# Kernel optimization log

Hardware: AMD Instinct MI355X
Metric: run time of the kernel (lower is better)

The kernel has to match this reference:

```python
import jax, jax.numpy as jnp
import numpy as np

B, D, L = 2048, 4096, 3
# Fixed 5-node star graph hardcoded in the source module
SRC = jnp.array([1, 2, 3, 4])
DST = jnp.array([0, 0, 0, 0])


def setup_inputs() -> dict:
    key = jax.random.key(0)
    ks = jax.random.split(key, 13)
    inp = {}
    names = ["pair_now", "person_1_now", "person_2_now", "scene_now",
             "pair_pre", "person_1_pre", "person_2_pre", "scene_pre"]
    for i, n in enumerate(names):
        inp[n] = jax.random.normal(ks[i], (B, D), dtype=jnp.float32)
    # GatedGraphConv per-layer message weight [L, D, D]
    inp["W"] = jax.random.normal(ks[8], (L, D, D), dtype=jnp.float32) * 0.02
    # GRUCell parameters (torch layout: [3D, D] for ih and hh, biases [3D])
    inp["w_ih"] = jax.random.normal(ks[9], (3 * D, D), dtype=jnp.float32) * 0.02
    inp["w_hh"] = jax.random.normal(ks[10], (3 * D, D), dtype=jnp.float32) * 0.02
    inp["b_ih"] = jax.random.normal(ks[11], (3 * D,), dtype=jnp.float32) * 0.02
    inp["b_hh"] = jax.random.normal(ks[12], (3 * D,), dtype=jnp.float32) * 0.02
    return inp


def _forward(pair_now, person_1_now, person_2_now, scene_now,
             pair_pre, person_1_pre, person_2_pre, scene_pre,
             W, w_ih, w_hh, b_ih, b_hh):
    # mean over batch dim -> one D-vector per stream
    pre_means = jnp.stack([pair_pre.mean(0), person_1_pre.mean(0),
                           person_2_pre.mean(0), scene_pre.mean(0)])  # [4, D]
    now_means = jnp.stack([pair_now.mean(0), person_1_now.mean(0),
                           person_2_now.mean(0), scene_now.mean(0)])  # [4, D]

    def ggc(node0):
        # node features: [node0, pair_pre, p1_pre, p2_pre, scene_pre] -> [5, D]
        h = jnp.concatenate([node0[None], pre_means], axis=0)

        def step(h, Wl):
            msg = h @ Wl                                   # [5, D]
            agg = jnp.zeros_like(h).at[DST].add(msg[SRC])  # star: sum into node 0
            # torch GRUCell
            gi = agg @ w_ih.T + b_ih                       # [5, 3D]
            gh = h @ w_hh.T + b_hh
            i_r, i_z, i_n = jnp.split(gi, 3, axis=-1)
            h_r, h_z, h_n = jnp.split(gh, 3, axis=-1)
            r = jax.nn.sigmoid(i_r + h_r)
            z = jax.nn.sigmoid(i_z + h_z)
            n = jnp.tanh(i_n + r * h_n)
            return (1.0 - z) * n + z * h, None

        h, _ = jax.lax.scan(step, h, W)
        return h[0]  # node-0 output [D]

    outs = jax.vmap(ggc)(now_means)                 # [4, D]
    losses = jnp.mean((outs - pre_means) ** 2, -1)  # MSE per stream
    return jnp.sum(losses) * 10.0


def reference(pair_now, person_1_now, person_2_now, scene_now,
              pair_pre, person_1_pre, person_2_pre, scene_pre,
              W, w_ih, w_hh, b_ih, b_hh):
    return _forward(pair_now, person_1_now, person_2_now, scene_now,
                    pair_pre, person_1_pre, person_2_pre, scene_pre,
                    W, w_ih, w_hh, b_ih, b_hh)
```

## Files before the change

kernel.cpp:

```cpp
#include <hip/hip_runtime.h>
#include <hip/hip_bf16.h>

#define B  2048
#define D  4096
#define D3 12288
#define L  3
#define BK 256

struct Ptrs8 { const float* p[8]; };

typedef float          f32x4 __attribute__((ext_vector_type(4)));
typedef unsigned int   u32x2 __attribute__((ext_vector_type(2)));
typedef unsigned short u16x4 __attribute__((ext_vector_type(4)));

__device__ __forceinline__ f32x4 ldnt4(const float* p) {
    return __builtin_nontemporal_load(reinterpret_cast<const f32x4*>(p));
}
__device__ __forceinline__ f32x4 ld4(const float* p) {
    return *reinterpret_cast<const f32x4*>(p);
}
__device__ __forceinline__ void gload16(const void* g, void* l) {
    __builtin_amdgcn_global_load_lds(
        (const __attribute__((address_space(1))) unsigned int*)g,
        (__attribute__((address_space(3))) unsigned int*)l, 16, 0, 0);
}

__device__ __forceinline__ unsigned short f2bf(float f) {
    union { float f; unsigned int u; } v; v.f = f;
    unsigned int r = v.u + 0x7FFFu + ((v.u >> 16) & 1u);
    return (unsigned short)(r >> 16);
}
__device__ __forceinline__ float bf_lo(unsigned int u) {
    union { unsigned int u; float f; } v; v.u = u << 16; return v.f;
}
__device__ __forceinline__ float bf_hi(unsigned int u) {
    union { unsigned int u; float f; } v; v.u = u & 0xFFFF0000u; return v.f;
}

__global__ void k_mean_partial(Ptrs8 in, float* __restrict__ partials) {
    const int cc = blockIdx.x, rc = blockIdx.y, m = blockIdx.z;
    const float* __restrict__ src = in.p[m];
    const int col0 = cc * 1024 + threadIdx.x * 4;
    const size_t base = (size_t)(rc * 32) * D + col0;
    f32x4 a0 = {0,0,0,0}, a1 = {0,0,0,0}, a2 = {0,0,0,0}, a3 = {0,0,0,0};
    #pragma unroll
    for (int r = 0; r < 32; r += 4) {
        a0 += ldnt4(src + base + (size_t)(r + 0) * D);
        a1 += ldnt4(src + base + (size_t)(r + 1) * D);
        a2 += ldnt4(src + base + (size_t)(r + 2) * D);
        a3 += ldnt4(src + base + (size_t)(r + 3) * D);
    }
    const f32x4 acc = (a0 + a1) + (a2 + a3);
    *reinterpret_cast<f32x4*>(partials + ((size_t)(m * 64 + rc)) * D + col0) = acc;
}

__global__ void k_mean_finalize(const float* __restrict__ partials,
                                float* __restrict__ means,
                                float* __restrict__ h,
                                float* __restrict__ svec) {
    const int d = blockIdx.x * 256 + threadIdx.x;
    float mv[8];
    #pragma unroll
    for (int m = 0; m < 8; ++m) {
        float s = 0.f;
        for (int rc = 0; rc < 64; ++rc) s += partials[(size_t)(m * 64 + rc) * D + d];
        mv[m] = s * (1.0f / (float)B);
        means[m * D + d] = mv[m];
    }
    float ssum = 0.f;
    #pragma unroll
    for (int j = 0; j < 4; ++j) {
        h[j * D + d] = mv[4 + j];
        ssum += mv[4 + j];
    }
    #pragma unroll
    for (int s = 0; s < 4; ++s)
        h[(4 + s) * D + d] = mv[s];
    svec[d] = ssum;
}

__global__ void k_aggmsg_partial(const float* __restrict__ Wl,
                                 const float* __restrict__ svec,
                                 float* __restrict__ partials) {
    const int col0 = blockIdx.x * 1024 + threadIdx.x * 4;
    const int row0 = blockIdx.y * 16;
    f32x4 a0 = {0,0,0,0}, a1 = {0,0,0,0}, a2 = {0,0,0,0}, a3 = {0,0,0,0};
    #pragma unroll
    for (int r = 0; r < 16; r += 4) {
        a0 += svec[row0 + r + 0] * ldnt4(Wl + (size_t)(row0 + r + 0) * D + col0);
        a1 += svec[row0 + r + 1] * ldnt4(Wl + (size_t)(row0 + r + 1) * D + col0);
        a2 += svec[row0 + r + 2] * ldnt4(Wl + (size_t)(row0 + r + 2) * D + col0);
        a3 += svec[row0 + r + 3] * ldnt4(Wl + (size_t)(row0 + r + 3) * D + col0);
    }
    const f32x4 acc = (a0 + a1) + (a2 + a3);
    *reinterpret_cast<f32x4*>(partials + (size_t)blockIdx.y * D + col0) = acc;
}

__global__ void k_aggmsg_reduce(const float* __restrict__ partials,
                                float* __restrict__ aggmsg) {
    const int d = blockIdx.x * 256 + threadIdx.x;
    float s = 0.f;
    for (int r = 0; r < 256; ++r) s += partials[(size_t)r * D + d];
    aggmsg[d] = s;
}

__global__ __launch_bounds__(256)
void k_gates_f32(const float* __restrict__ w_ih,
                 const float* __restrict__ w_hh,
                 const float* __restrict__ h,
                 const float* __restrict__ aggmsg,
                 const float* __restrict__ b_ih,
                 const float* __restrict__ b_hh,
                 float* __restrict__ gi0,
                 float* __restrict__ gh,
                 unsigned short* __restrict__ wih_bf,
                 unsigned short* __restrict__ whh_bf) {
    __shared__ float sw[2][16][BK];
    const bool is_ih = (blockIdx.x >= 768);
    const int  kbase = (is_ih ? blockIdx.x - 768 : blockIdx.x) * 16;
    const float* __restrict__ wsrc = is_ih ? w_ih : w_hh;
    unsigned short* __restrict__ wdst = is_ih ? wih_bf : whh_bf;
    const int wid = threadIdx.x >> 6, lane = threadIdx.x & 63;

    auto stage = [&](int t, int b) {
        #pragma unroll
        for (int rr = 0; rr < 4; ++rr) {
            const int row = wid * 4 + rr;
            gload16(wsrc + (size_t)(kbase + row) * D + t * BK + lane * 4,
                    &sw[b][row][0]);
        }
    };

    float acc[4][8] = {};
    stage(0, 0);
    __syncthreads();
    for (int t = 0; t < 16; ++t) {
        if (t + 1 < 16) stage(t + 1, (t + 1) & 1);
        const int cb = t & 1;
        f32x4 wreg[4];
        #pragma unroll
        for (int rr = 0; rr < 4; ++rr) {
            const int row = wid * 4 + rr;
            wreg[rr] = *reinterpret_cast<const f32x4*>(&sw[cb][row][lane * 4]);
            u16x4 wb;
            wb.x = f2bf(wreg[rr].x); wb.y = f2bf(wreg[rr].y);
            wb.z = f2bf(wreg[rr].z); wb.w = f2bf(wreg[rr].w);
            *reinterpret_cast<u16x4*>(
                wdst + (size_t)(kbase + row) * D + t * BK + lane * 4) = wb;
        }
        if (!is_ih) {
            #pragma unroll
            for (int j = 0; j < 8; ++j) {
                const f32x4 hv = ld4(h + j * D + t * BK + lane * 4);
                #pragma unroll
                for (int rr = 0; rr < 4; ++rr)
                    acc[rr][j] += wreg[rr].x * hv.x + wreg[rr].y * hv.y
                                + wreg[rr].z * hv.z + wreg[rr].w * hv.w;
            }
        } else {
            const f32x4 av = ld4(aggmsg + t * BK + lane * 4);
            #pragma unroll
            for (int rr = 0; rr < 4; ++rr)
                acc[rr][0] += wreg[rr].x * av.x + wreg[rr].y * av.y
                            + wreg[rr].z * av.z + wreg[rr].w * av.w;
        }
        __syncthreads();
    }

    if (!is_ih) {
        #pragma unroll
        for (int rr = 0; rr < 4; ++rr)
            #pragma unroll
            for (int j = 0; j < 8; ++j) {
                float v = acc[rr][j];
                #pragma unroll
                for (int off = 32; off; off >>= 1) v += __shfl_xor(v, off);
                if (lane == 0)
                    gh[(size_t)j * D3 + kbase + wid * 4 + rr] = v + b_hh[kbase + wid * 4 + rr];
            }
    } else {
        #pragma unroll
        for (int rr = 0; rr < 4; ++rr) {
            float v = acc[rr][0];
            #pragma unroll
            for (int off = 32; off; off >>= 1) v += __shfl_xor(v, off);
            if (lane == 0)
                gi0[kbase + wid * 4 + rr] = v + b_ih[kbase + wid * 4 + rr];
        }
    }
}

__global__ __launch_bounds__(256)
void k_gates_bf(const unsigned short* __restrict__ wih_bf,
                const unsigned short* __restrict__ whh_bf,
                const float* __restrict__ h,
                const float* __restrict__ aggmsg,
                const float* __restrict__ b_ih,
                const float* __restrict__ b_hh,
                float* __restrict__ gi0,
                float* __restrict__ gh) {
    __shared__ unsigned short sw[2][16][BK];
    const bool is_ih = (blockIdx.x >= 768);
    const int  kbase = (is_ih ? blockIdx.x - 768 : blockIdx.x) * 16;
    const unsigned short* __restrict__ wsrc = is_ih ? wih_bf : whh_bf;
    const int wid = threadIdx.x >> 6, lane = threadIdx.x & 63;

    auto stage = [&](int t, int b) {
        #pragma unroll
        for (int c = 0; c < 2; ++c) {
            const int row = wid * 4 + c * 2;
            gload16(wsrc + (size_t)(kbase + row + (lane >> 5)) * D
                         + t * BK + (lane & 31) * 8,
                    &sw[b][row][0]);
        }
    };

    float acc[4][8] = {};
    stage(0, 0);
    __syncthreads();
    for (int t = 0; t < 16; ++t) {
        if (t + 1 < 16) stage(t + 1, (t + 1) & 1);
        const int cb = t & 1;
        float wf[4][4];
        #pragma unroll
        for (int rr = 0; rr < 4; ++rr) {
            const u32x2 wu = *reinterpret_cast<const u32x2*>(
                &sw[cb][wid * 4 + rr][lane * 4]);
            wf[rr][0] = bf_lo(wu.x); wf[rr][1] = bf_hi(wu.x);
            wf[rr][2] = bf_lo(wu.y); wf[rr][3] = bf_hi(wu.y);
        }
        if (!is_ih) {
            #pragma unroll
            for (int j = 0; j < 8; ++j) {
                const f32x4 hv = ld4(h + j * D + t * BK + lane * 4);
                #pragma unroll
                for (int rr = 0; rr < 4; ++rr)
                    acc[rr][j] += wf[rr][0] * hv.x + wf[rr][1] * hv.y
                                + wf[rr][2] * hv.z + wf[rr][3] * hv.w;
            }
        } else {
            const f32x4 av = ld4(aggmsg + t * BK + lane * 4);
            #pragma unroll
            for (int rr = 0; rr < 4; ++rr)
                acc[rr][0] += wf[rr][0] * av.x + wf[rr][1] * av.y
                            + wf[rr][2] * av.z + wf[rr][3] * av.w;
        }
        __syncthreads();
    }

    if (!is_ih) {
        #pragma unroll
        for (int rr = 0; rr < 4; ++rr)
            #pragma unroll
            for (int j = 0; j < 8; ++j) {
                float v = acc[rr][j];
                #pragma unroll
                for (int off = 32; off; off >>= 1) v += __shfl_xor(v, off);
                if (lane == 0)
                    gh[(size_t)j * D3 + kbase + wid * 4 + rr] = v + b_hh[kbase + wid * 4 + rr];
            }
    } else {
        #pragma unroll
        for (int rr = 0; rr < 4; ++rr) {
            float v = acc[rr][0];
            #pragma unroll
            for (int off = 32; off; off >>= 1) v += __shfl_xor(v, off);
            if (lane == 0)
                gi0[kbase + wid * 4 + rr] = v + b_ih[kbase + wid * 4 + rr];
        }
    }
}

__device__ __forceinline__ float sigmoidf_(float x) {
    return 1.0f / (1.0f + __expf(-x));
}

__global__ void k_gru(const float* __restrict__ gi0,
                      const float* __restrict__ gh,
                      const float* __restrict__ b_ih,
                      float* __restrict__ h,
                      float* __restrict__ svec) {
    const int d = blockIdx.x * 256 + threadIdx.x;
    const float bir = b_ih[d], biz = b_ih[D + d], bin = b_ih[2 * D + d];
    const float gir = gi0[d],  giz = gi0[D + d],  gin = gi0[2 * D + d];
    float ssum = 0.f;
    #pragma unroll
    for (int j = 0; j < 8; ++j) {
        const float ir = (j < 4) ? bir : gir;
        const float iz = (j < 4) ? biz : giz;
        const float in = (j < 4) ? bin : gin;
        const float hr = gh[(size_t)j * D3 + d];
        const float hz = gh[(size_t)j * D3 + D + d];
        const float hn = gh[(size_t)j * D3 + 2 * D + d];
        const float hv = h[j * D + d];
        const float r = sigmoidf_(ir + hr);
        const float z = sigmoidf_(iz + hz);
        const float n = tanhf(in + r * hn);
        const float hnew = (1.f - z) * n + z * hv;
        h[j * D + d] = hnew;
        if (j < 4) ssum += hnew;
    }
    svec[d] = ssum;
}

__global__ void k_loss(const float* __restrict__ h,
                       const float* __restrict__ means,
                       float* __restrict__ out) {
    __shared__ float red[4];
    float acc = 0.f;
    for (int idx = threadIdx.x; idx < 4 * D; idx += 256) {
        const int s = idx >> 12;
        const int d = idx & (D - 1);
        const float diff = h[(4 + s) * D + d] - means[(4 + s) * D + d];
        acc += diff * diff;
    }
    #pragma unroll
    for (int off = 32; off; off >>= 1) acc += __shfl_xor(acc, off);
    const int wave = threadIdx.x >> 6, lane = threadIdx.x & 63;
    if (lane == 0) red[wave] = acc;
    __syncthreads();
    if (threadIdx.x == 0)
        out[0] = (red[0] + red[1] + red[2] + red[3]) * (10.0f / (float)D);
}

extern "C" void kernel_launch(void* const* d_in, const int* in_sizes, int n_in,
                              void* d_out, int out_size, void* d_ws, size_t ws_size,
                              hipStream_t stream) {
    const float* W    = (const float*)d_in[8];
    const float* w_ih = (const float*)d_in[9];
    const float* w_hh = (const float*)d_in[10];
    const float* b_ih = (const float*)d_in[11];
    const float* b_hh = (const float*)d_in[12];

    float* ws     = (float*)d_ws;
    float* mpart  = ws;
    float* means  = mpart  + 8 * 64 * D;
    float* h      = means  + 8 * D;
    float* svec   = h      + 8 * D;
    float* apart  = svec   + D;
    float* aggmsg = apart  + 256 * D;
    float* gi0    = aggmsg + D;
    float* gh     = gi0    + D3;
    float* wbase  = gh     + 8 * D3;
    unsigned short* wih_bf = (unsigned short*)wbase;
    unsigned short* whh_bf = wih_bf + (size_t)D3 * D;

    Ptrs8 in8;
    for (int i = 0; i < 8; ++i) in8.p[i] = (const float*)d_in[i];

    k_mean_partial<<<dim3(4, 64, 8), 256, 0, stream>>>(in8, mpart);
    k_mean_finalize<<<16, 256, 0, stream>>>(mpart, means, h, svec);

    for (int l = 0; l < L; ++l) {
        const float* Wl = W + (size_t)l * D * D;
        k_aggmsg_partial<<<dim3(4, 256), 256, 0, stream>>>(Wl, svec, apart);
        k_aggmsg_reduce<<<16, 256, 0, stream>>>(apart, aggmsg);
        if (l == 0)
            k_gates_f32<<<1536, 256, 0, stream>>>(w_ih, w_hh, h, aggmsg,
                                                  b_ih, b_hh, gi0, gh,
                                                  wih_bf, whh_bf);
        else
            k_gates_bf<<<1536, 256, 0, stream>>>(wih_bf, whh_bf, h, aggmsg,
                                                 b_ih, b_hh, gi0, gh);
        k_gru<<<16, 256, 0, stream>>>(gi0, gh, b_ih, h, svec);
    }

    k_loss<<<1, 256, 0, stream>>>(h, means, (float*)d_out);
}
```

Before: 397.5 us.

## Restructure GRU gate GEMV kernels to direct register loads with rebalanced work split

Replaces the LDS double-buffered staging (global_load_lds plus __syncthreads) in both gate kernels with direct vector loads of weights into registers. w_hh blocks now cover 8 rows with each wave handling 2 of the 8 batch vectors, and w_ih rows get their own 384 blocks of 32 rows, for a grid of 1920. The bf16 kernel reads 8 bf16 values per lane per load, and conversion uses the HIP __float22bfloat162_rn intrinsic. The goal is to remove barrier and LDS overhead and rebalance the ih and hh halves. In exchange, the h vectors and w_hh rows are re-read by every wave, which adds cache traffic.

```diff
diff --git a/kernel.cpp b/kernel.cpp
--- a/kernel.cpp
+++ b/kernel.cpp
@@ -5,13 +5,12 @@
 #define D  4096
 #define D3 12288
 #define L  3
-#define BK 256
 
 struct Ptrs8 { const float* p[8]; };
 
 typedef float          f32x4 __attribute__((ext_vector_type(4)));
 typedef unsigned int   u32x2 __attribute__((ext_vector_type(2)));
-typedef unsigned short u16x4 __attribute__((ext_vector_type(4)));
+typedef unsigned int   u32x4 __attribute__((ext_vector_type(4)));
 
 __device__ __forceinline__ f32x4 ldnt4(const float* p) {
     return __builtin_nontemporal_load(reinterpret_cast<const f32x4*>(p));
@@ -19,22 +18,20 @@
 __device__ __forceinline__ f32x4 ld4(const float* p) {
     return *reinterpret_cast<const f32x4*>(p);
 }
-__device__ __forceinline__ void gload16(const void* g, void* l) {
-    __builtin_amdgcn_global_load_lds(
-        (const __attribute__((address_space(1))) unsigned int*)g,
-        (__attribute__((address_space(3))) unsigned int*)l, 16, 0, 0);
-}
-
-__device__ __forceinline__ unsigned short f2bf(float f) {
-    union { float f; unsigned int u; } v; v.f = f;
-    unsigned int r = v.u + 0x7FFFu + ((v.u >> 16) & 1u);
-    return (unsigned short)(r >> 16);
-}
 __device__ __forceinline__ float bf_lo(unsigned int u) {
     union { unsigned int u; float f; } v; v.u = u << 16; return v.f;
 }
 __device__ __forceinline__ float bf_hi(unsigned int u) {
     union { unsigned int u; float f; } v; v.u = u & 0xFFFF0000u; return v.f;
+}
+__device__ __forceinline__ void st_bf16x4(unsigned short* dst, f32x4 w) {
+    __hip_bfloat162 p0 = __float22bfloat162_rn(make_float2(w.x, w.y));
+    __hip_bfloat162 p1 = __float22bfloat162_rn(make_float2(w.z, w.w));
+    unsigned int u0, u1;
+    __builtin_memcpy(&u0, &p0, 4);
+    __builtin_memcpy(&u1, &p1, 4);
+    u32x2 v; v.x = u0; v.y = u1;
+    *reinterpret_cast<u32x2*>(dst) = v;
 }
 
 __global__ void k_mean_partial(Ptrs8 in, float* __restrict__ partials) {
@@ -115,77 +112,63 @@
                  float* __restrict__ gh,
                  unsigned short* __restrict__ wih_bf,
                  unsigned short* __restrict__ whh_bf) {
-    __shared__ float sw[2][16][BK];
-    const bool is_ih = (blockIdx.x >= 768);
-    const int  kbase = (is_ih ? blockIdx.x - 768 : blockIdx.x) * 16;
-    const float* __restrict__ wsrc = is_ih ? w_ih : w_hh;
-    unsigned short* __restrict__ wdst = is_ih ? wih_bf : whh_bf;
     const int wid = threadIdx.x >> 6, lane = threadIdx.x & 63;
-
-    auto stage = [&](int t, int b) {
+    if (blockIdx.x < 1536) {
+        const int kbase = blockIdx.x * 8;
+        const int j0 = wid * 2;
+        float acc[8][2] = {};
+        for (int i = 0; i < 16; ++i) {
+            const int idx = i * 256 + lane * 4;
+            const f32x4 hv0 = ld4(h + j0 * D + idx);
+            const f32x4 hv1 = ld4(h + (j0 + 1) * D + idx);
+            f32x4 w[8];
+            #pragma unroll
+            for (int r = 0; r < 8; ++r)
+                w[r] = ld4(w_hh + (size_t)(kbase + r) * D + idx);
+            st_bf16x4(whh_bf + (size_t)(kbase + j0) * D + idx, w[j0]);
+            st_bf16x4(whh_bf + (size_t)(kbase + j0 + 1) * D + idx, w[j0 + 1]);
+            #pragma unroll
+            for (int r = 0; r < 8; ++r) {
+                acc[r][0] += w[r].x * hv0.x + w[r].y * hv0.y
+                           + w[r].z * hv0.z + w[r].w * hv0.w;
+                acc[r][1] += w[r].x * hv1.x + w[r].y * hv1.y
+                           + w[r].z * hv1.z + w[r].w * hv1.w;
+            }
+        }
         #pragma unroll
-        for (int rr = 0; rr < 4; ++rr) {
-            const int row = wid * 4 + rr;
-            gload16(wsrc + (size_t)(kbase + row) * D + t * BK + lane * 4,
-                    &sw[b][row][0]);
-        }
-    };
-
-    float acc[4][8] = {};
-    stage(0, 0);
-    __syncthreads();
-    for (int t = 0; t < 16; ++t) {
-        if (t + 1 < 16) stage(t + 1, (t + 1) & 1);
-        const int cb = t & 1;
-        f32x4 wreg[4];
-        #pragma unroll
-        for (int rr = 0; rr < 4; ++rr) {
-            const int row = wid * 4 + rr;
-            wreg[rr] = *reinterpret_cast<const f32x4*>(&sw[cb][row][lane * 4]);
-            u16x4 wb;
-            wb.x = f2bf(wreg[rr].x); wb.y = f2bf(wreg[rr].y);
-            wb.z = f2bf(wreg[rr].z); wb.w = f2bf(wreg[rr].w);
-            *reinterpret_cast<u16x4*>(
-                wdst + (size_t)(kbase + row) * D + t * BK + lane * 4) = wb;
-        }
-        if (!is_ih) {
-            #pragma unroll
-            for (int j = 0; j < 8; ++j) {
-                const f32x4 hv = ld4(h + j * D + t * BK + lane * 4);
-                #pragma unroll
-                for (int rr = 0; rr < 4; ++rr)
-                    acc[rr][j] += wreg[rr].x * hv.x + wreg[rr].y * hv.y
-                                + wreg[rr].z * hv.z + wreg[rr].w * hv.w;
-            }
-        } else {
-            const f32x4 av = ld4(aggmsg + t * BK + lane * 4);
-            #pragma unroll
-            for (int rr = 0; rr < 4; ++rr)
-                acc[rr][0] += wreg[rr].x * av.x + wreg[rr].y * av.y
-                            + wreg[rr].z * av.z + wreg[rr].w * av.w;
-        }
-        __syncthreads();
-    }
-
-    if (!is_ih) {
-        #pragma unroll
-        for (int rr = 0; rr < 4; ++rr)
-            #pragma unroll
-            for (int j = 0; j < 8; ++j) {
-                float v = acc[rr][j];
+        for (int r = 0; r < 8; ++r)
+            #pragma unroll
+            for (int jj = 0; jj < 2; ++jj) {
+                float v = acc[r][jj];
                 #pragma unroll
                 for (int off = 32; off; off >>= 1) v += __shfl_xor(v, off);
                 if (lane == 0)
-                    gh[(size_t)j * D3 + kbase + wid * 4 + rr] = v + b_hh[kbase + wid * 4 + rr];
+                    gh[(size_t)(j0 + jj) * D3 + kbase + r] = v + b_hh[kbase + r];
             }
     } else {
+        const int k0 = (blockIdx.x - 1536) * 32 + wid * 8;
+        float acc[8] = {};
+        for (int i = 0; i < 16; ++i) {
+            const int idx = i * 256 + lane * 4;
+            const f32x4 av = ld4(aggmsg + idx);
+            f32x4 w[8];
+            #pragma unroll
+            for (int r = 0; r < 8; ++r)
+                w[r] = ld4(w_ih + (size_t)(k0 + r) * D + idx);
+            #pragma unroll
+            for (int r = 0; r < 8; ++r)
+                st_bf16x4(wih_bf + (size_t)(k0 + r) * D + idx, w[r]);
+            #pragma unroll
+            for (int r = 0; r < 8; ++r)
+                acc[r] += w[r].x * av.x + w[r].y * av.y
+                        + w[r].z * av.z + w[r].w * av.w;
+        }
         #pragma unroll
-        for (int rr = 0; rr < 4; ++rr) {
-            float v = acc[rr][0];
+        for (int r = 0; r < 8; ++r) {
+            float v = acc[r];
             #pragma unroll
             for (int off = 32; off; off >>= 1) v += __shfl_xor(v, off);
-            if (lane == 0)
-                gi0[kbase + wid * 4 + rr] = v + b_ih[kbase + wid * 4 + rr];
+            if (lane == 0) gi0[k0 + r] = v + b_ih[k0 + r];
         }
     }
 }
@@ -199,74 +182,69 @@
                 const float* __restrict__ b_hh,
                 float* __restrict__ gi0,
                 float* __restrict__ gh) {
-    __shared__ unsigned short sw[2][16][BK];
-    const bool is_ih = (blockIdx.x >= 768);
-    const int  kbase = (is_ih ? blockIdx.x - 768 : blockIdx.x) * 16;
-    const unsigned short* __restrict__ wsrc = is_ih ? wih_bf : whh_bf;
     const int wid = threadIdx.x >> 6, lane = threadIdx.x & 63;
-
-    auto stage = [&](int t, int b) {
+    if (blockIdx.x < 1536) {
+        const int kbase = blockIdx.x * 8;
+        const int j0 = wid * 2;
+        float acc[8][2] = {};
+        for (int i = 0; i < 8; ++i) {
+            const int idx = i * 512 + lane * 8;
+            const f32x4 h0a = ld4(h + j0 * D + idx);
+            const f32x4 h0b = ld4(h + j0 * D + idx + 4);
+            const f32x4 h1a = ld4(h + (j0 + 1) * D + idx);
+            const f32x4 h1b = ld4(h + (j0 + 1) * D + idx + 4);
+            u32x4 w[8];
+            #pragma unroll
+            for (int r = 0; r < 8; ++r)
+                w[r] = *reinterpret_cast<const u32x4*>(
+                    whh_bf + (size_t)(kbase + r) * D + idx);
+            #pragma unroll
+            for (int r = 0; r < 8; ++r) {
+                const float f0 = bf_lo(w[r].x), f1 = bf_hi(w[r].x);
+                const float f2 = bf_lo(w[r].y), f3 = bf_hi(w[r].y);
+                const float f4 = bf_lo(w[r].z), f5 = bf_hi(w[r].z);
+                const float f6 = bf_lo(w[r].w), f7 = bf_hi(w[r].w);
+                acc[r][0] += f0 * h0a.x + f1 * h0a.y + f2 * h0a.z + f3 * h0a.w
+                           + f4 * h0b.x + f5 * h0b.y + f6 * h0b.z + f7 * h0b.w;
+                acc[r][1] += f0 * h1a.x + f1 * h1a.y + f2 * h1a.z + f3 * h1a.w
+                           + f4 * h1b.x + f5 * h1b.y + f6 * h1b.z + f7 * h1b.w;
+            }
+        }
         #pragma unroll
-        for (int c = 0; c < 2; ++c) {
-            const int row = wid * 4 + c * 2;
-            gload16(wsrc + (size_t)(kbase + row + (lane >> 5)) * D
-                         + t * BK + (lane & 31) * 8,
-                    &sw[b][row][0]);
-        }
-    };
-
-    float acc[4][8] = {};
-    stage(0, 0);
-    __syncthreads();
-    for (int t = 0; t < 16; ++t) {
-        if (t + 1 < 16) stage(t + 1, (t + 1) & 1);
-        const int cb = t & 1;
-        float wf[4][4];
-        #pragma unroll
-        for (int rr = 0; rr < 4; ++rr) {
-            const u32x2 wu = *reinterpret_cast<const u32x2*>(
-                &sw[cb][wid * 4 + rr][lane * 4]);
-            wf[rr][0] = bf_lo(wu.x); wf[rr][1] = bf_hi(wu.x);
-            wf[rr][2] = bf_lo(wu.y); wf[rr][3] = bf_hi(wu.y);
-        }
-        if (!is_ih) {
-            #pragma unroll
-            for (int j = 0; j < 8; ++j) {
-                const f32x4 hv = ld4(h + j * D + t * BK + lane * 4);
-                #pragma unroll
-                for (int rr = 0; rr < 4; ++rr)
-                    acc[rr][j] += wf[rr][0] * hv.x + wf[rr][1] * hv.y
-                                + wf[rr][2] * hv.z + wf[rr][3] * hv.w;
-            }
-        } else {
-            const f32x4 av = ld4(aggmsg + t * BK + lane * 4);
-            #pragma unroll
-            for (int rr = 0; rr < 4; ++rr)
-                acc[rr][0] += wf[rr][0] * av.x + wf[rr][1] * av.y
-                            + wf[rr][2] * av.z + wf[rr][3] * av.w;
-        }
-        __syncthreads();
-    }
-
-    if (!is_ih) {
-        #pragma unroll
-        for (int rr = 0; rr < 4; ++rr)
-            #pragma unroll
-            for (int j = 0; j < 8; ++j) {
-                float v = acc[rr][j];
+        for (int r = 0; r < 8; ++r)
+            #pragma unroll
+            for (int jj = 0; jj < 2; ++jj) {
+                float v = acc[r][jj];
                 #pragma unroll
                 for (int off = 32; off; off >>= 1) v += __shfl_xor(v, off);
                 if (lane == 0)
-                    gh[(size_t)j * D3 + kbase + wid * 4 + rr] = v + b_hh[kbase + wid * 4 + rr];
+                    gh[(size_t)(j0 + jj) * D3 + kbase + r] = v + b_hh[kbase + r];
             }
     } else {
+        const int k0 = (blockIdx.x - 1536) * 32 + wid * 8;
+        float acc[8] = {};
+        for (int i = 0; i < 8; ++i) {
+            const int idx = i * 512 + lane * 8;
+            const f32x4 a0 = ld4(aggmsg + idx);
+            const f32x4 a1 = ld4(aggmsg + idx + 4);
+            u32x4 w[8];
+            #pragma unroll
+            for (int r = 0; r < 8; ++r)
+                w[r] = *reinterpret_cast<const u32x4*>(
+                    wih_bf + (size_t)(k0 + r) * D + idx);
+            #pragma unroll
+            for (int r = 0; r < 8; ++r)
+                acc[r] += bf_lo(w[r].x) * a0.x + bf_hi(w[r].x) * a0.y
+                        + bf_lo(w[r].y) * a0.z + bf_hi(w[r].y) * a0.w
+                        + bf_lo(w[r].z) * a1.x + bf_hi(w[r].z) * a1.y
+                        + bf_lo(w[r].w) * a1.z + bf_hi(w[r].w) * a1.w;
+        }
         #pragma unroll
-        for (int rr = 0; rr < 4; ++rr) {
-            float v = acc[rr][0];
+        for (int r = 0; r < 8; ++r) {
+            float v = acc[r];
             #pragma unroll
             for (int off = 32; off; off >>= 1) v += __shfl_xor(v, off);
-            if (lane == 0)
-                gi0[kbase + wid * 4 + rr] = v + b_ih[kbase + wid * 4 + rr];
+            if (lane == 0) gi0[k0 + r] = v + b_ih[k0 + r];
         }
     }
 }
@@ -356,11 +334,11 @@
         k_aggmsg_partial<<<dim3(4, 256), 256, 0, stream>>>(Wl, svec, apart);
         k_aggmsg_reduce<<<16, 256, 0, stream>>>(apart, aggmsg);
         if (l == 0)
-            k_gates_f32<<<1536, 256, 0, stream>>>(w_ih, w_hh, h, aggmsg,
+            k_gates_f32<<<1920, 256, 0, stream>>>(w_ih, w_hh, h, aggmsg,
                                                   b_ih, b_hh, gi0, gh,
                                                   wih_bf, whh_bf);
         else
-            k_gates_bf<<<1536, 256, 0, stream>>>(wih_bf, whh_bf, h, aggmsg,
+            k_gates_bf<<<1920, 256, 0, stream>>>(wih_bf, whh_bf, h, aggmsg,
                                                  b_ih, b_hh, gi0, gh);
         k_gru<<<16, 256, 0, stream>>>(gi0, gh, b_ih, h, svec);
     }
```

After: 504.7 us. 26.9% more time.
